# Kernel optimization log

Measured on AMD Instinct MI355X. Metric: run time of the kernel, lower is better.

Reference implementation:

```python
import jax, jax.numpy as jnp
import numpy as np

B, S, H = 2, 1024, 2048
KD = 32
N_CACHE = 16
RANKS = (4, 12, 40, 128)
SIM_THRESH = 0.95
CRIT_T, SIMPLE_T = 0.8, 0.3
EPS = 1e-8


def setup_inputs() -> dict:
    key = jax.random.key(0)
    ks = jax.random.split(key, 24)
    f32 = jnp.float32
    inp = {}
    inp['hidden_states'] = jax.random.normal(ks[0], (B, S, H), f32)
    # token importance scorer: Linear(H, H//4) -> ReLU -> Linear(H//4, 1)
    inp['scorer_w1'] = jax.random.normal(ks[1], (H // 4, H), f32) * 0.1
    inp['scorer_b1'] = jnp.zeros((H // 4,), f32)
    inp['scorer_w2'] = jax.random.normal(ks[2], (1, H // 4), f32) * 0.1
    inp['scorer_b2'] = jnp.zeros((1,), f32)
    inp['pos_importance'] = jnp.ones((1024,), f32)
    # orthogonal key projection [KD, H] (rows orthonormal)
    q, _ = jnp.linalg.qr(jax.random.normal(ks[3], (H, KD), f32))
    inp['key_proj_w'] = q.T
    # cached keys: per-batch-row L2-normalized then flattened, as in _compute_key
    ck = jax.random.normal(ks[4], (N_CACHE, B, KD), f32)
    ck = ck / jnp.linalg.norm(ck, axis=-1, keepdims=True)
    inp['cache_keys'] = ck.reshape(N_CACHE, B * KD)
    inp['cache_deltas'] = jax.random.normal(ks[5], (N_CACHE, B, S, H), f32) * 0.02
    # complexity estimator: Linear(H, 64) -> ReLU -> Linear(64, 4)
    inp['ce_w1'] = jax.random.normal(ks[6], (64, H), f32) * 0.02
    inp['ce_b1'] = jnp.zeros((64,), f32)
    inp['ce_w2'] = jax.random.normal(ks[7], (len(RANKS), 64), f32) * 0.02
    inp['ce_b2'] = jnp.zeros((len(RANKS),), f32)
    # adaptive low-rank U/V per rank option, init std=0.02
    for i, r in enumerate(RANKS):
        inp[f'u{r}'] = jax.random.normal(ks[8 + 2 * i], (r, H), f32) * 0.02
        inp[f'v{r}'] = jax.random.normal(ks[9 + 2 * i], (H, r), f32) * 0.02
    # dense stand-in for the wrapped original transformer layer
    inp['layer_w'] = jax.random.normal(ks[16], (H, H), f32) * 0.02
    inp['layer_b'] = jnp.zeros((H,), f32)
    return inp


def _forward(hidden_states, scorer_w1, scorer_b1, scorer_w2, scorer_b2,
             pos_importance, key_proj_w, cache_keys, cache_deltas,
             ce_w1, ce_b1, ce_w2, ce_b2,
             u4, v4, u12, v12, u40, v40, u128, v128,
             layer_w, layer_b):
    x = hidden_states
    Bn, Sn, _ = x.shape
    # ---- token importance scoring ----
    h = jax.nn.relu(jnp.einsum('bsh,fh->bsf', x, scorer_w1) + scorer_b1)
    content = jnp.einsum('bsf,of->bso', h, scorer_w2)[..., 0] + scorer_b2[0]  # [B,S]
    pos = pos_importance[:Sn][None, :]
    imp = jax.nn.sigmoid(content + 0.1 * pos)
    imp = imp.at[:, 0].multiply(2.0).at[:, -1].multiply(2.0)
    critical = imp > CRIT_T
    simple = imp < SIMPLE_T
    normal = ~(critical | simple)
    # ---- critical path: original layer on critically-masked input ----
    crit_in = jnp.where(critical[..., None], x, 0.0)
    crit_out = jnp.einsum('bsh,oh->bso', crit_in, layer_w) + layer_b
    # ---- simple path: batched 1-NN cosine cache lookup (replaces python loop) ----
    x_pooled = x.mean(axis=1)  # [B,H]
    qk = jax.lax.stop_gradient(x_pooled @ key_proj_w.T)  # no_grad in original
    qk = qk / jnp.maximum(jnp.linalg.norm(qk, axis=-1, keepdims=True), EPS)
    qf = qk.reshape(-1)  # flattened [B*KD], as F.cosine_similarity(dim=0)
    ck = jax.lax.stop_gradient(cache_keys)  # cached entries are detached
    sims = (ck @ qf) / (jnp.maximum(jnp.linalg.norm(ck, axis=-1), EPS)
                        * jnp.maximum(jnp.linalg.norm(qf), EPS))  # [N_CACHE]
    best = jnp.argmax(sims)
    hit = sims[best] >= SIM_THRESH
    cached_delta = jax.lax.stop_gradient(cache_deltas[best])  # [B,S,H]
    lr4 = (x @ u4.T) @ v4.T  # rank-4 update on cache miss
    simple_out = x + jnp.where(hit, cached_delta, lr4)
    # ---- normal path: adaptive-rank low-rank update ----
    ce_h = jax.nn.relu(jax.lax.stop_gradient(x_pooled) @ ce_w1.T + ce_b1)
    scores = ce_h @ ce_w2.T + ce_b2  # [B,4]
    rank_idx = jnp.argmax(scores.reshape(-1)) % len(RANKS)  # flat argmax as torch.argmax
    branches = [
        lambda xx: (xx @ u4.T) @ v4.T,
        lambda xx: (xx @ u12.T) @ v12.T,
        lambda xx: (xx @ u40.T) @ v40.T,
        lambda xx: (xx @ u128.T) @ v128.T,
    ]
    normal_update = jax.lax.switch(rank_idx, branches, x)
    normal_out = x + normal_update
    # ---- route per-token (masks partition all tokens) ----
    out = jnp.where(critical[..., None], crit_out,
          jnp.where(simple[..., None], simple_out, normal_out))
    return out


def reference(hidden_states, scorer_w1, scorer_b1, scorer_w2, scorer_b2,
              pos_importance, key_proj_w, cache_keys, cache_deltas,
              ce_w1, ce_b1, ce_w2, ce_b2,
              u4, v4, u12, v12, u40, v40, u128, v128,
              layer_w, layer_b):
    return _forward(hidden_states, scorer_w1, scorer_b1, scorer_w2, scorer_b2,
                    pos_importance, key_proj_w, cache_keys, cache_deltas,
                    ce_w1, ce_b1, ce_w2, ce_b2,
                    u4, v4, u12, v12, u40, v40, u128, v128,
                    layer_w, layer_b)
```

## Files before the change

### kernel.cpp

```cpp
#include <hip/hip_runtime.h>
#include <math.h>

#define B_  2
#define S_  1024
#define H_  2048
#define F_  512
#define KD_ 32
#define NC_ 16
#define M_  2048
#define NPROJ 184
#define LDP 192
#define KZ_ 4

typedef __attribute__((ext_vector_type(8))) short bf16x8;
typedef __attribute__((ext_vector_type(4))) float f32x4;

typedef __attribute__((address_space(1))) const void gvoid_t;
typedef __attribute__((address_space(3))) void lvoid_t;

__device__ __forceinline__ void gld16(const void* g, void* l) {
    __builtin_amdgcn_global_load_lds((gvoid_t*)g, (lvoid_t*)l, 16, 0, 0);
}

__device__ __forceinline__ ushort f2bf(float f) {
    unsigned u = __float_as_uint(f);
    u += 0x7FFFu + ((u >> 16) & 1u);
    return (ushort)(u >> 16);
}
__device__ __forceinline__ float bf2f(ushort h) {
    return __uint_as_float(((unsigned)h) << 16);
}
__device__ __forceinline__ uint4 pack_hi8(float4 a, float4 b) {
    uint4 r;
    r.x = (unsigned)f2bf(a.x) | ((unsigned)f2bf(a.y) << 16);
    r.y = (unsigned)f2bf(a.z) | ((unsigned)f2bf(a.w) << 16);
    r.z = (unsigned)f2bf(b.x) | ((unsigned)f2bf(b.y) << 16);
    r.w = (unsigned)f2bf(b.z) | ((unsigned)f2bf(b.w) << 16);
    return r;
}
__device__ __forceinline__ void pack_hilo8(float4 a, float4 b, uint4* hi, uint4* lo) {
    float v[8] = {a.x, a.y, a.z, a.w, b.x, b.y, b.z, b.w};
    unsigned h[8], l[8];
#pragma unroll
    for (int i = 0; i < 8; ++i) {
        ushort hh = f2bf(v[i]);
        h[i] = hh;
        l[i] = f2bf(v[i] - bf2f(hh));
    }
    *hi = make_uint4(h[0] | (h[1] << 16), h[2] | (h[3] << 16),
                     h[4] | (h[5] << 16), h[6] | (h[7] << 16));
    *lo = make_uint4(l[0] | (l[1] << 16), l[2] | (l[3] << 16),
                     l[4] | (l[5] << 16), l[6] | (l[7] << 16));
}

__global__ __launch_bounds__(256) void conv_kernel(
    const float* __restrict__ x, const float* __restrict__ lw,
    const float* __restrict__ sw1,
    const float* __restrict__ u4, const float* __restrict__ u12,
    const float* __restrict__ u40, const float* __restrict__ u128,
    ushort* __restrict__ xhi, ushort* __restrict__ xlo,
    ushort* __restrict__ lwh, ushort* __restrict__ swh,
    ushort* __restrict__ swl, ushort* __restrict__ ubh,
    float* __restrict__ partial) {
    int blk = blockIdx.x, tid = threadIdx.x;
    if (blk < 128) {
        int c0 = tid << 3;
        float cs0 = 0.f, cs1 = 0.f, cs2 = 0.f, cs3 = 0.f;
        float cs4 = 0.f, cs5 = 0.f, cs6 = 0.f, cs7 = 0.f;
        for (int r = 0; r < 16; ++r) {
            size_t off = (size_t)(blk * 16 + r) * H_ + c0;
            float4 a = *(const float4*)(x + off);
            float4 b = *(const float4*)(x + off + 4);
            cs0 += a.x; cs1 += a.y; cs2 += a.z; cs3 += a.w;
            cs4 += b.x; cs5 += b.y; cs6 += b.z; cs7 += b.w;
            uint4 hi, lo;
            pack_hilo8(a, b, &hi, &lo);
            *(uint4*)(xhi + off) = hi;
            *(uint4*)(xlo + off) = lo;
        }
        float* pr = partial + (size_t)blk * H_ + c0;
        pr[0] = cs0; pr[1] = cs1; pr[2] = cs2; pr[3] = cs3;
        pr[4] = cs4; pr[5] = cs5; pr[6] = cs6; pr[7] = cs7;
    } else if (blk < 1152) {
        size_t base = (size_t)(blk - 128) * 4096 + (size_t)tid * 16;
#pragma unroll
        for (int q = 0; q < 2; ++q) {
            size_t o = base + q * 8;
            float4 a = *(const float4*)(lw + o);
            float4 b = *(const float4*)(lw + o + 4);
            *(uint4*)(lwh + o) = pack_hi8(a, b);
        }
    } else if (blk < 1408) {
        size_t base = (size_t)(blk - 1152) * 4096 + (size_t)tid * 16;
#pragma unroll
        for (int q = 0; q < 2; ++q) {
            size_t o = base + q * 8;
            float4 a = *(const float4*)(sw1 + o);
            float4 b = *(const float4*)(sw1 + o + 4);
            uint4 hi, lo;
            pack_hilo8(a, b, &hi, &lo);
            *(uint4*)(swh + o) = hi;
            *(uint4*)(swl + o) = lo;
        }
    } else {
        const float* src; ushort* dst; int rel;
        if (blk < 1410)      { src = u4;   dst = ubh;            rel = blk - 1408; }
        else if (blk < 1416) { src = u12;  dst = ubh + 4 * H_;   rel = blk - 1410; }
        else if (blk < 1436) { src = u40;  dst = ubh + 16 * H_;  rel = blk - 1416; }
        else                 { src = u128; dst = ubh + 56 * H_;  rel = blk - 1436; }
        size_t base = (size_t)rel * 4096 + (size_t)tid * 16;
#pragma unroll
        for (int q = 0; q < 2; ++q) {
            size_t o = base + q * 8;
            float4 a = *(const float4*)(src + o);
            float4 b = *(const float4*)(src + o + 4);
            *(uint4*)(dst + o) = pack_hi8(a, b);
        }
    }
}

__global__ __launch_bounds__(256) void pooldots_kernel(
    const float* __restrict__ partial, const float* __restrict__ kpw,
    const float* __restrict__ cw1, float* __restrict__ dots) {
    __shared__ float red[4];
    int o = blockIdx.x, tid = threadIdx.x;
    int b; const float* wr;
    if (o < 64) {
        b = o >> 5;
        wr = kpw + (size_t)(o & 31) * H_;
    } else {
        int o2 = o - 64;
        b = o2 >> 6;
        wr = cw1 + (size_t)(o2 & 63) * H_;
    }
    int k0 = tid << 3;
    float xs0 = 0.f, xs1 = 0.f, xs2 = 0.f, xs3 = 0.f;
    float xs4 = 0.f, xs5 = 0.f, xs6 = 0.f, xs7 = 0.f;
    const float* pb = partial + (size_t)b * 64 * H_ + k0;
    for (int seg = 0; seg < 64; ++seg) {
        float4 p0 = *(const float4*)(pb + (size_t)seg * H_);
        float4 p1 = *(const float4*)(pb + (size_t)seg * H_ + 4);
        xs0 += p0.x; xs1 += p0.y; xs2 += p0.z; xs3 += p0.w;
        xs4 += p1.x; xs5 += p1.y; xs6 += p1.z; xs7 += p1.w;
    }
    const float inv = 1.0f / S_;
    float4 wa = *(const float4*)(wr + k0);
    float4 wb = *(const float4*)(wr + k0 + 4);
    float s = (xs0 * inv) * wa.x + (xs1 * inv) * wa.y
            + (xs2 * inv) * wa.z + (xs3 * inv) * wa.w
            + (xs4 * inv) * wb.x + (xs5 * inv) * wb.y
            + (xs6 * inv) * wb.z + (xs7 * inv) * wb.w;
    for (int off = 32; off > 0; off >>= 1) s += __shfl_down(s, off, 64);
    if ((tid & 63) == 0) red[tid >> 6] = s;
    __syncthreads();
    if (tid == 0) dots[o] = red[0] + red[1] + red[2] + red[3];
}

__global__ __launch_bounds__(256) void big_gemm(
    const ushort* __restrict__ xhi, const ushort* __restrict__ xlo,
    const ushort* __restrict__ swh, const ushort* __restrict__ swl,
    const ushort* __restrict__ ubh,
    float* __restrict__ Hp, float* __restrict__ Pp) {
    __shared__ ushort Ah[2][128][32], Al[2][128][32], Bh[2][128][32], Bl[2][128][32];
    int m0 = blockIdx.x << 7;
    int ny = blockIdx.y;
    int kz = blockIdx.z;
    bool split = ny < 4;
    int tid = threadIdx.x;
    int lr = tid >> 2;
    int lc = (tid & 3) << 3;
    int lcs = lc ^ (((lr >> 1) & 3) << 3);

    const ushort* a0p = xhi + (size_t)(m0 + lr) * H_ + lcs;
    const ushort* a1p = a0p + (size_t)64 * H_;
    const ushort* l0p = xlo + (size_t)(m0 + lr) * H_ + lcs;
    const ushort* l1p = l0p + (size_t)64 * H_;
    const ushort* b0p; const ushort* b1p;
    const ushort* c0p = l0p; const ushort* c1p = l1p;
    if (split) {
        b0p = swh + (size_t)(ny * 128 + lr) * H_ + lcs;
        b1p = b0p + (size_t)64 * H_;
        c0p = swl + (size_t)(ny * 128 + lr) * H_ + lcs;
        c1p = c0p + (size_t)64 * H_;
    } else {
        b0p = ubh + (size_t)((ny - 4) * 128 + lr) * H_ + lcs;
        b1p = b0p + (size_t)64 * H_;
    }

    int lane = tid & 63, w = tid >> 6;
    int wm = (w >> 1) << 6, wn = (w & 1) << 6;
    int fr = lane & 15;
    int kb = ((lane >> 4) << 3) ^ (((fr >> 1) & 3) << 3);

    f32x4 zero4 = {0.f, 0.f, 0.f, 0.f};
    f32x4 acc[4][4];
#pragma unroll
    for (int i = 0; i < 4; ++i)
#pragma unroll
        for (int j = 0; j < 4; ++j) acc[i][j] = zero4;

    int kbeg = kz << 9;

#define STAGE_BG(bb, k0)                                                  \
    do {                                                                  \
        gld16(a0p + (k0), &Ah[bb][lr][lc]);                               \
        gld16(a1p + (k0), &Ah[bb][lr + 64][lc]);                          \
        gld16(b0p + (k0), &Bh[bb][lr][lc]);                               \
        gld16(b1p + (k0), &Bh[bb][lr + 64][lc]);                          \
        if (split) {                                                      \
            gld16(l0p + (k0), &Al[bb][lr][lc]);                           \
            gld16(l1p + (k0), &Al[bb][lr + 64][lc]);                      \
            gld16(c0p + (k0), &Bl[bb][lr][lc]);                           \
            gld16(c1p + (k0), &Bl[bb][lr + 64][lc]);                      \
        }                                                                 \
    } while (0)

    STAGE_BG(0, kbeg);
    __syncthreads();
    int cur = 0;
    for (int kt = 0; kt < 16; ++kt) {
        if (kt + 1 < 16) STAGE_BG(cur ^ 1, kbeg + ((kt + 1) << 5));
        bf16x8 ah[4], bh4[4], al4[4], bl4[4];
#pragma unroll
        for (int mt = 0; mt < 4; ++mt)
            ah[mt] = *(const bf16x8*)&Ah[cur][wm + (mt << 4) + fr][kb];
#pragma unroll
        for (int nt = 0; nt < 4; ++nt)
            bh4[nt] = *(const bf16x8*)&Bh[cur][wn + (nt << 4) + fr][kb];
        if (split) {
#pragma unroll
            for (int mt = 0; mt < 4; ++mt)
                al4[mt] = *(const bf16x8*)&Al[cur][wm + (mt << 4) + fr][kb];
#pragma unroll
            for (int nt = 0; nt < 4; ++nt)
                bl4[nt] = *(const bf16x8*)&Bl[cur][wn + (nt << 4) + fr][kb];
        }
#pragma unroll
        for (int mt = 0; mt < 4; ++mt)
#pragma unroll
            for (int nt = 0; nt < 4; ++nt) {
                acc[mt][nt] = __builtin_amdgcn_mfma_f32_16x16x32_bf16(
                    ah[mt], bh4[nt], acc[mt][nt], 0, 0, 0);
                if (split) {
                    acc[mt][nt] = __builtin_amdgcn_mfma_f32_16x16x32_bf16(
                        ah[mt], bl4[nt], acc[mt][nt], 0, 0, 0);
                    acc[mt][nt] = __builtin_amdgcn_mfma_f32_16x16x32_bf16(
                        al4[mt], bh4[nt], acc[mt][nt], 0, 0, 0);
                }
            }
        __syncthreads();
        cur ^= 1;
    }
#undef STAGE_BG

    int orr = (lane >> 4) << 2;
    if (split) {
        float* dst = Hp + (size_t)kz * M_ * F_;
#pragma unroll
        for (int mt = 0; mt < 4; ++mt)
#pragma unroll
            for (int r = 0; r < 4; ++r) {
                int m = m0 + wm + (mt << 4) + orr + r;
                float* cr = dst + (size_t)m * F_ + (ny << 7) + wn;
#pragma unroll
                for (int nt = 0; nt < 4; ++nt)
                    cr[(nt << 4) + fr] = acc[mt][nt][r];
            }
    } else {
        float* dst = Pp + (size_t)kz * M_ * LDP;
        int nb0 = (ny - 4) << 7;
#pragma unroll
        for (int mt = 0; mt < 4; ++mt)
#pragma unroll
            for (int r = 0; r < 4; ++r) {
                int m = m0 + wm + (mt << 4) + orr + r;
                float* cr = dst + (size_t)m * LDP;
#pragma unroll
                for (int nt = 0; nt < 4; ++nt) {
                    int c = nb0 + wn + (nt << 4) + fr;
                    if (c < NPROJ) cr[c] = acc[mt][nt][r];
                }
            }
    }
}

__global__ __launch_bounds__(256) void routefinal_kernel(
    const float* __restrict__ Hp, const float* __restrict__ sb1,
    const float* __restrict__ sw2, const float* __restrict__ sb2,
    const float* __restrict__ pos,
    const float* __restrict__ dots, const float* __restrict__ ck,
    const float* __restrict__ cb1, const float* __restrict__ cw2,
    const float* __restrict__ cb2,
    int* __restrict__ flags, int* __restrict__ route, int* __restrict__ clist) {
    int tid = threadIdx.x;
    if (blockIdx.x < 512) {
        int m = ((int)blockIdx.x << 2) + (tid >> 6);
        int lane = tid & 63;
        const float* h0 = Hp + (size_t)m * F_;
        const float* h1 = h0 + (size_t)M_ * F_;
        const float* h2 = h1 + (size_t)M_ * F_;
        const float* h3 = h2 + (size_t)M_ * F_;
        float s = 0.f;
        for (int f = lane; f < F_; f += 64)
            s += fmaxf(h0[f] + h1[f] + h2[f] + h3[f] + sb1[f], 0.f) * sw2[f];
        for (int off = 32; off > 0; off >>= 1) s += __shfl_down(s, off, 64);
        if (lane == 0) {
            float content = s + sb2[0];
            int si = m & (S_ - 1);
            float imp = 1.0f / (1.0f + expf(-(content + 0.1f * pos[si])));
            if (si == 0 || si == S_ - 1) imp *= 2.0f;
            int rt = (imp > 0.8f) ? 0 : ((imp < 0.3f) ? 1 : 2);
            route[m] = rt;
            if (rt == 0) {
                int idx = atomicAdd(&flags[0], 1);
                clist[idx] = m;
            }
        }
        return;
    }
    __shared__ float qk_s[64], ce_s[128], sims_s[NC_], sc_s[8];
    __shared__ float qn_s;
    if (tid < 64) {
        qk_s[tid]      = dots[tid];
        ce_s[tid]      = fmaxf(dots[64 + tid] + cb1[tid & 63], 0.f);
        ce_s[tid + 64] = fmaxf(dots[128 + tid] + cb1[tid & 63], 0.f);
    }
    __syncthreads();
    if (tid == 0) {
        for (int b = 0; b < B_; ++b) {
            float nn = 0.f;
            for (int d = 0; d < KD_; ++d) { float v = qk_s[b * KD_ + d]; nn += v * v; }
            float den = fmaxf(sqrtf(nn), 1e-8f);
            for (int d = 0; d < KD_; ++d) qk_s[b * KD_ + d] /= den;
        }
        float qn = 0.f;
        for (int i = 0; i < B_ * KD_; ++i) qn += qk_s[i] * qk_s[i];
        qn_s = fmaxf(sqrtf(qn), 1e-8f);
    }
    __syncthreads();
    if (tid < NC_) {
        float dot = 0.f, nn = 0.f;
        for (int i = 0; i < B_ * KD_; ++i) {
            float c = ck[tid * (B_ * KD_) + i];
            dot += c * qk_s[i]; nn += c * c;
        }
        sims_s[tid] = dot / (fmaxf(sqrtf(nn), 1e-8f) * qn_s);
    }
    if (tid >= 32 && tid < 40) {
        int p = tid - 32, b = p >> 2, o = p & 3;
        float v = cb2[o];
        for (int j = 0; j < 64; ++j) v += ce_s[b * 64 + j] * cw2[o * 64 + j];
        sc_s[p] = v;
    }
    __syncthreads();
    if (tid == 0) {
        float bestv = -1e30f; int best = 0;
        for (int n = 0; n < NC_; ++n)
            if (sims_s[n] > bestv) { bestv = sims_s[n]; best = n; }
        flags[2] = (bestv >= 0.95f) ? 1 : 0;
        flags[3] = best;
        float bs = -1e30f; int bi = 0;
        for (int p = 0; p < 8; ++p)
            if (sc_s[p] > bs) { bs = sc_s[p]; bi = p; }
        flags[1] = bi & 3;
    }
}

__global__ __launch_bounds__(256) void critstage2_kernel(
    const ushort* __restrict__ xhi, const ushort* __restrict__ lwh,
    const float* __restrict__ lb,
    const float* __restrict__ x, const float* __restrict__ Pp,
    const float* __restrict__ v4, const float* __restrict__ v12,
    const float* __restrict__ v40, const float* __restrict__ v128,
    const float* __restrict__ cd, const int* __restrict__ flags,
    const int* __restrict__ route, const int* __restrict__ clist,
    float* __restrict__ out) {
    __shared__ __align__(16) char smem[32768];
    int bi = blockIdx.x;
    int tid = threadIdx.x;

    if (bi < 256) {
        ushort* As = (ushort*)smem;
        ushort* Bs = As + 8192;
        int M = flags[0];
        int m0 = (bi >> 4) << 7;
        if (m0 >= M) return;
        int n0 = (bi & 15) << 7;
        int lr = tid >> 2, lc = (tid & 3) << 3;
        int lcs = lc ^ (((lr >> 1) & 3) << 3);

        int gm0 = m0 + lr, gm1 = m0 + lr + 64;
        int ar0 = clist[gm0 < M ? gm0 : (M - 1)];
        int ar1 = clist[gm1 < M ? gm1 : (M - 1)];
        const ushort* a0p = xhi + (size_t)ar0 * H_ + lcs;
        const ushort* a1p = xhi + (size_t)ar1 * H_ + lcs;
        const ushort* b0p = lwh + (size_t)(n0 + lr) * H_ + lcs;
        const ushort* b1p = b0p + (size_t)64 * H_;

        int lane = tid & 63, w = tid >> 6;
        int wm = (w >> 1) << 6, wn = (w & 1) << 6;
        int fr = lane & 15;
        int kb = ((lane >> 4) << 3) ^ (((fr >> 1) & 3) << 3);

        f32x4 zero4 = {0.f, 0.f, 0.f, 0.f};
        f32x4 acc[4][4];
#pragma unroll
        for (int i = 0; i < 4; ++i)
#pragma unroll
            for (int j = 0; j < 4; ++j) acc[i][j] = zero4;

#define STAGE_CG(bb, k0)                                                  \
        do {                                                              \
            gld16(a0p + (k0), &As[(bb) * 4096 + lr * 32 + lc]);           \
            gld16(a1p + (k0), &As[(bb) * 4096 + (lr + 64) * 32 + lc]);    \
            gld16(b0p + (k0), &Bs[(bb) * 4096 + lr * 32 + lc]);           \
            gld16(b1p + (k0), &Bs[(bb) * 4096 + (lr + 64) * 32 + lc]);    \
        } while (0)

        STAGE_CG(0, 0);
        __syncthreads();
        int cur = 0;
        for (int kt = 0; kt < 64; ++kt) {
            if (kt + 1 < 64) STAGE_CG(cur ^ 1, (kt + 1) << 5);
            bf16x8 af[4], bf4[4];
#pragma unroll
            for (int mt = 0; mt < 4; ++mt)
                af[mt] = *(const bf16x8*)&As[cur * 4096 + (wm + (mt << 4) + fr) * 32 + kb];
#pragma unroll
            for (int nt = 0; nt < 4; ++nt)
                bf4[nt] = *(const bf16x8*)&Bs[cur * 4096 + (wn + (nt << 4) + fr) * 32 + kb];
#pragma unroll
            for (int mt = 0; mt < 4; ++mt)
#pragma unroll
                for (int nt = 0; nt < 4; ++nt)
                    acc[mt][nt] = __builtin_amdgcn_mfma_f32_16x16x32_bf16(
                        af[mt], bf4[nt], acc[mt][nt], 0, 0, 0);
            __syncthreads();
            cur ^= 1;
        }
#undef STAGE_CG

        int orr = (lane >> 4) << 2;
#pragma unroll
        for (int mt = 0; mt < 4; ++mt)
#pragma unroll
            for (int r = 0; r < 4; ++r) {
                int m = m0 + wm + (mt << 4) + orr + r;
                if (m < M) {
                    float* cr = out + (size_t)clist[m] * H_;
#pragma unroll
                    for (int nt = 0; nt < 4; ++nt) {
                        int c = n0 + wn + (nt << 4) + fr;
                        cr[c] = acc[mt][nt][r] + lb[c];
                    }
                }
            }
        return;
    }

    float* TsR = (float*)smem;
    float* Ts4 = TsR + 16 * 132;
    int*   rt_s = (int*)(Ts4 + 64);
    int sb = bi - 256;
    int m0 = (sb >> 4) << 4;
    int c0 = (sb & 15) << 7;

    if (tid < 16) rt_s[tid] = route[m0 + tid];
    int r = flags[1];
    const float* V = (r == 0) ? v4 : (r == 1) ? v12 : (r == 2) ? v40 : v128;
    int Kr  = (r == 0) ? 4 : (r == 1) ? 12 : (r == 2) ? 40 : 128;
    int off = (r == 0) ? 0 : (r == 1) ? 4  : (r == 2) ? 16 : 56;
    int hit = flags[2], best = flags[3];

    const float* Pp1 = Pp + (size_t)M_ * LDP;
    const float* Pp2 = Pp1 + (size_t)M_ * LDP;
    const float* Pp3 = Pp2 + (size_t)M_ * LDP;
    for (int idx = tid; idx < 16 * Kr; idx += 256) {
        int i = idx / Kr, j = idx - i * Kr;
        size_t o = (size_t)(m0 + i) * LDP + off + j;
        TsR[i * 132 + j] = Pp[o] + Pp1[o] + Pp2[o] + Pp3[o];
    }
    if (tid < 64) {
        int i = tid >> 2, j = tid & 3;
        size_t o = (size_t)(m0 + i) * LDP + j;
        Ts4[i * 4 + j] = Pp[o] + Pp1[o] + Pp2[o] + Pp3[o];
    }
    __syncthreads();
    bool any1 = false, any2 = false;
#pragma unroll
    for (int i = 0; i < 16; ++i) { any1 |= (rt_s[i] == 1); any2 |= (rt_s[i] == 2); }
    if (!any1 && !any2) return;
    bool need4 = any1 && !hit;

    int c = c0 + (tid & 127);
    int i0 = (tid >> 7) << 3;

    float aR[8];
#pragma unroll
    for (int i = 0; i < 8; ++i) aR[i] = 0.f;
    if (any2) {
        const float* vrow = V + (size_t)c * Kr;
        for (int j = 0; j < Kr; j += 4) {
            const float4 vv = *(const float4*)(vrow + j);
#pragma unroll
            for (int i = 0; i < 8; ++i) {
                const float4 tv = *(const float4*)&TsR[(i0 + i) * 132 + j];
                aR[i] += tv.x * vv.x + tv.y * vv.y + tv.z * vv.z + tv.w * vv.w;
            }
        }
    }
    float a4[8];
    if (need4) {
        const float4 vv = *(const float4*)(v4 + (size_t)c * 4);
#pragma unroll
        for (int i = 0; i < 8; ++i) {
            const float4 tv = *(const float4*)&Ts4[(i0 + i) * 4];
            a4[i] = tv.x * vv.x + tv.y * vv.y + tv.z * vv.z + tv.w * vv.w;
        }
    }
#pragma unroll
    for (int i = 0; i < 8; ++i) {
        int rt = rt_s[i0 + i];
        if (rt == 0) continue;
        size_t o = (size_t)(m0 + i0 + i) * H_ + c;
        float upd;
        if (rt == 1)
            upd = hit ? cd[(size_t)best * (size_t)(M_ * H_) + o] : a4[i];
        else
            upd = aR[i];
        out[o] = x[o] + upd;
    }
}

extern "C" void kernel_launch(void* const* d_in, const int* in_sizes, int n_in,
                              void* d_out, int out_size, void* d_ws, size_t ws_size,
                              hipStream_t stream) {
    const float* x    = (const float*)d_in[0];
    const float* sw1  = (const float*)d_in[1];
    const float* sb1  = (const float*)d_in[2];
    const float* sw2  = (const float*)d_in[3];
    const float* sb2  = (const float*)d_in[4];
    const float* pos  = (const float*)d_in[5];
    const float* kpw  = (const float*)d_in[6];
    const float* ck   = (const float*)d_in[7];
    const float* cd   = (const float*)d_in[8];
    const float* cw1  = (const float*)d_in[9];
    const float* cb1  = (const float*)d_in[10];
    const float* cw2  = (const float*)d_in[11];
    const float* cb2  = (const float*)d_in[12];
    const float* u4   = (const float*)d_in[13];
    const float* v4   = (const float*)d_in[14];
    const float* u12  = (const float*)d_in[15];
    const float* v12  = (const float*)d_in[16];
    const float* u40  = (const float*)d_in[17];
    const float* v40  = (const float*)d_in[18];
    const float* u128 = (const float*)d_in[19];
    const float* v128 = (const float*)d_in[20];
    const float* lw   = (const float*)d_in[21];
    const float* lb   = (const float*)d_in[22];
    float* out = (float*)d_out;

    ushort* xhi = (ushort*)d_ws;
    ushort* xlo = xhi + (size_t)M_ * H_;
    ushort* lwh = xlo + (size_t)M_ * H_;
    ushort* swh = lwh + (size_t)H_ * H_;
    ushort* swl = swh + (size_t)F_ * H_;
    ushort* ubh = swl + (size_t)F_ * H_;
    float* fbase   = (float*)(ubh + (size_t)256 * H_);
    float* partial = fbase;
    float* Pp      = partial + 128 * H_;
    float* Hp      = Pp + (size_t)KZ_ * M_ * LDP;
    float* dots    = Hp + (size_t)KZ_ * M_ * F_;
    int*   flags   = (int*)(dots + 256);
    int*   route   = flags + 8;
    int*   clist   = route + M_;

    hipMemsetAsync(flags, 0, sizeof(int), stream);

    conv_kernel<<<1500, 256, 0, stream>>>(x, lw, sw1, u4, u12, u40, u128,
                                          xhi, xlo, lwh, swh, swl, ubh, partial);
    pooldots_kernel<<<192, 256, 0, stream>>>(partial, kpw, cw1, dots);
    big_gemm<<<dim3(16, 6, KZ_), 256, 0, stream>>>(xhi, xlo, swh, swl, ubh, Hp, Pp);
    routefinal_kernel<<<513, 256, 0, stream>>>(Hp, sb1, sw2, sb2, pos,
                                               dots, ck, cb1, cw2, cb2,
                                               flags, route, clist);
    critstage2_kernel<<<2304, 256, 0, stream>>>(xhi, lwh, lb, x, Pp,
                                                v4, v12, v40, v128,
                                                cd, flags, route, clist, out);
}
```

Baseline: 479.6 us.

## Fold pooldots into big_gemm, drop memset, widen stage-2 low-rank tiles

The memset of the flag word moves into conv_kernel, and the pooled-dot work is folded into big_gemm as an extra grid row (ny==6). Each of those blocks computes three dot outputs, which removes two launches and lets the dot work run alongside the GEMM. The low-rank stage-2 blocks now cover 256 columns instead of 128, halving their count. They also check the route early, so blocks with no work exit before loading the Pp partial sums into shared memory. The trade-off is fewer blocks in stage 2 and a few slower extra blocks in the GEMM grid.

```diff
diff --git a/kernel.cpp b/kernel.cpp
--- a/kernel.cpp
+++ b/kernel.cpp
@@ -61,8 +61,9 @@
     ushort* __restrict__ xhi, ushort* __restrict__ xlo,
     ushort* __restrict__ lwh, ushort* __restrict__ swh,
     ushort* __restrict__ swl, ushort* __restrict__ ubh,
-    float* __restrict__ partial) {
+    float* __restrict__ partial, int* __restrict__ flags) {
     int blk = blockIdx.x, tid = threadIdx.x;
+    if (blk == 0 && tid == 0) flags[0] = 0;
     if (blk < 128) {
         int c0 = tid << 3;
         float cs0 = 0.f, cs1 = 0.f, cs2 = 0.f, cs3 = 0.f;
@@ -119,54 +120,61 @@
     }
 }
 
-__global__ __launch_bounds__(256) void pooldots_kernel(
-    const float* __restrict__ partial, const float* __restrict__ kpw,
-    const float* __restrict__ cw1, float* __restrict__ dots) {
-    __shared__ float red[4];
-    int o = blockIdx.x, tid = threadIdx.x;
-    int b; const float* wr;
-    if (o < 64) {
-        b = o >> 5;
-        wr = kpw + (size_t)(o & 31) * H_;
-    } else {
-        int o2 = o - 64;
-        b = o2 >> 6;
-        wr = cw1 + (size_t)(o2 & 63) * H_;
-    }
-    int k0 = tid << 3;
-    float xs0 = 0.f, xs1 = 0.f, xs2 = 0.f, xs3 = 0.f;
-    float xs4 = 0.f, xs5 = 0.f, xs6 = 0.f, xs7 = 0.f;
-    const float* pb = partial + (size_t)b * 64 * H_ + k0;
-    for (int seg = 0; seg < 64; ++seg) {
-        float4 p0 = *(const float4*)(pb + (size_t)seg * H_);
-        float4 p1 = *(const float4*)(pb + (size_t)seg * H_ + 4);
-        xs0 += p0.x; xs1 += p0.y; xs2 += p0.z; xs3 += p0.w;
-        xs4 += p1.x; xs5 += p1.y; xs6 += p1.z; xs7 += p1.w;
-    }
-    const float inv = 1.0f / S_;
-    float4 wa = *(const float4*)(wr + k0);
-    float4 wb = *(const float4*)(wr + k0 + 4);
-    float s = (xs0 * inv) * wa.x + (xs1 * inv) * wa.y
-            + (xs2 * inv) * wa.z + (xs3 * inv) * wa.w
-            + (xs4 * inv) * wb.x + (xs5 * inv) * wb.y
-            + (xs6 * inv) * wb.z + (xs7 * inv) * wb.w;
-    for (int off = 32; off > 0; off >>= 1) s += __shfl_down(s, off, 64);
-    if ((tid & 63) == 0) red[tid >> 6] = s;
-    __syncthreads();
-    if (tid == 0) dots[o] = red[0] + red[1] + red[2] + red[3];
-}
-
 __global__ __launch_bounds__(256) void big_gemm(
     const ushort* __restrict__ xhi, const ushort* __restrict__ xlo,
     const ushort* __restrict__ swh, const ushort* __restrict__ swl,
     const ushort* __restrict__ ubh,
-    float* __restrict__ Hp, float* __restrict__ Pp) {
+    const float* __restrict__ partial, const float* __restrict__ kpw,
+    const float* __restrict__ cw1,
+    float* __restrict__ Hp, float* __restrict__ Pp, float* __restrict__ dots) {
     __shared__ ushort Ah[2][128][32], Al[2][128][32], Bh[2][128][32], Bl[2][128][32];
-    int m0 = blockIdx.x << 7;
+    __shared__ float red_s[4];
     int ny = blockIdx.y;
     int kz = blockIdx.z;
+    int tid = threadIdx.x;
+
+    if (ny == 6) {
+        int idx = ((int)blockIdx.x << 2) | kz;
+        int k0 = tid << 3;
+        const float inv = 1.0f / S_;
+#pragma unroll
+        for (int t = 0; t < 3; ++t) {
+            int o = idx + t * 64;
+            int b; const float* wr;
+            if (o < 64) {
+                b = o >> 5;
+                wr = kpw + (size_t)(o & 31) * H_;
+            } else {
+                int o2 = o - 64;
+                b = o2 >> 6;
+                wr = cw1 + (size_t)(o2 & 63) * H_;
+            }
+            float xs0 = 0.f, xs1 = 0.f, xs2 = 0.f, xs3 = 0.f;
+            float xs4 = 0.f, xs5 = 0.f, xs6 = 0.f, xs7 = 0.f;
+            const float* pb = partial + (size_t)b * 64 * H_ + k0;
+            for (int seg = 0; seg < 64; ++seg) {
+                float4 p0 = *(const float4*)(pb + (size_t)seg * H_);
+                float4 p1 = *(const float4*)(pb + (size_t)seg * H_ + 4);
+                xs0 += p0.x; xs1 += p0.y; xs2 += p0.z; xs3 += p0.w;
+                xs4 += p1.x; xs5 += p1.y; xs6 += p1.z; xs7 += p1.w;
+            }
+            float4 wa = *(const float4*)(wr + k0);
+            float4 wb = *(const float4*)(wr + k0 + 4);
+            float s = (xs0 * inv) * wa.x + (xs1 * inv) * wa.y
+                    + (xs2 * inv) * wa.z + (xs3 * inv) * wa.w
+                    + (xs4 * inv) * wb.x + (xs5 * inv) * wb.y
+                    + (xs6 * inv) * wb.z + (xs7 * inv) * wb.w;
+            for (int off = 32; off > 0; off >>= 1) s += __shfl_down(s, off, 64);
+            __syncthreads();
+            if ((tid & 63) == 0) red_s[tid >> 6] = s;
+            __syncthreads();
+            if (tid == 0) dots[o] = red_s[0] + red_s[1] + red_s[2] + red_s[3];
+        }
+        return;
+    }
+
+    int m0 = blockIdx.x << 7;
     bool split = ny < 4;
-    int tid = threadIdx.x;
     int lr = tid >> 2;
     int lc = (tid & 3) << 3;
     int lcs = lc ^ (((lr >> 1) & 3) << 3);
@@ -462,73 +470,80 @@
     float* Ts4 = TsR + 16 * 132;
     int*   rt_s = (int*)(Ts4 + 64);
     int sb = bi - 256;
-    int m0 = (sb >> 4) << 4;
-    int c0 = (sb & 15) << 7;
+    int m0 = (sb >> 3) << 4;
+    int c0 = (sb & 7) << 8;
 
     if (tid < 16) rt_s[tid] = route[m0 + tid];
+    __syncthreads();
+    bool any1 = false, any2 = false;
+#pragma unroll
+    for (int i = 0; i < 16; ++i) { any1 |= (rt_s[i] == 1); any2 |= (rt_s[i] == 2); }
+    if (!any1 && !any2) return;
+
     int r = flags[1];
     const float* V = (r == 0) ? v4 : (r == 1) ? v12 : (r == 2) ? v40 : v128;
     int Kr  = (r == 0) ? 4 : (r == 1) ? 12 : (r == 2) ? 40 : 128;
     int off = (r == 0) ? 0 : (r == 1) ? 4  : (r == 2) ? 16 : 56;
     int hit = flags[2], best = flags[3];
+    bool need4 = any1 && !hit;
 
     const float* Pp1 = Pp + (size_t)M_ * LDP;
     const float* Pp2 = Pp1 + (size_t)M_ * LDP;
     const float* Pp3 = Pp2 + (size_t)M_ * LDP;
-    for (int idx = tid; idx < 16 * Kr; idx += 256) {
-        int i = idx / Kr, j = idx - i * Kr;
-        size_t o = (size_t)(m0 + i) * LDP + off + j;
-        TsR[i * 132 + j] = Pp[o] + Pp1[o] + Pp2[o] + Pp3[o];
-    }
-    if (tid < 64) {
+    if (any2) {
+        for (int idx = tid; idx < 16 * Kr; idx += 256) {
+            int i = idx / Kr, j = idx - i * Kr;
+            size_t o = (size_t)(m0 + i) * LDP + off + j;
+            TsR[i * 132 + j] = Pp[o] + Pp1[o] + Pp2[o] + Pp3[o];
+        }
+    }
+    if (need4 && tid < 64) {
         int i = tid >> 2, j = tid & 3;
         size_t o = (size_t)(m0 + i) * LDP + j;
         Ts4[i * 4 + j] = Pp[o] + Pp1[o] + Pp2[o] + Pp3[o];
     }
     __syncthreads();
-    bool any1 = false, any2 = false;
-#pragma unroll
-    for (int i = 0; i < 16; ++i) { any1 |= (rt_s[i] == 1); any2 |= (rt_s[i] == 2); }
-    if (!any1 && !any2) return;
-    bool need4 = any1 && !hit;
-
-    int c = c0 + (tid & 127);
+
     int i0 = (tid >> 7) << 3;
-
-    float aR[8];
-#pragma unroll
-    for (int i = 0; i < 8; ++i) aR[i] = 0.f;
-    if (any2) {
-        const float* vrow = V + (size_t)c * Kr;
-        for (int j = 0; j < Kr; j += 4) {
-            const float4 vv = *(const float4*)(vrow + j);
+#pragma unroll
+    for (int hseg = 0; hseg < 2; ++hseg) {
+        int c = c0 + (hseg << 7) + (tid & 127);
+
+        float aR[8];
+#pragma unroll
+        for (int i = 0; i < 8; ++i) aR[i] = 0.f;
+        if (any2) {
+            const float* vrow = V + (size_t)c * Kr;
+            for (int j = 0; j < Kr; j += 4) {
+                const float4 vv = *(const float4*)(vrow + j);
+#pragma unroll
+                for (int i = 0; i < 8; ++i) {
+                    const float4 tv = *(const float4*)&TsR[(i0 + i) * 132 + j];
+                    aR[i] += tv.x * vv.x + tv.y * vv.y + tv.z * vv.z + tv.w * vv.w;
+                }
+            }
+        }
+        float a4[8];
+        if (need4) {
+            const float4 vv = *(const float4*)(v4 + (size_t)c * 4);
 #pragma unroll
             for (int i = 0; i < 8; ++i) {
-                const float4 tv = *(const float4*)&TsR[(i0 + i) * 132 + j];
-                aR[i] += tv.x * vv.x + tv.y * vv.y + tv.z * vv.z + tv.w * vv.w;
-            }
-        }
-    }
-    float a4[8];
-    if (need4) {
-        const float4 vv = *(const float4*)(v4 + (size_t)c * 4);
+                const float4 tv = *(const float4*)&Ts4[(i0 + i) * 4];
+                a4[i] = tv.x * vv.x + tv.y * vv.y + tv.z * vv.z + tv.w * vv.w;
+            }
+        }
 #pragma unroll
         for (int i = 0; i < 8; ++i) {
-            const float4 tv = *(const float4*)&Ts4[(i0 + i) * 4];
-            a4[i] = tv.x * vv.x + tv.y * vv.y + tv.z * vv.z + tv.w * vv.w;
-        }
-    }
-#pragma unroll
-    for (int i = 0; i < 8; ++i) {
-        int rt = rt_s[i0 + i];
-        if (rt == 0) continue;
-        size_t o = (size_t)(m0 + i0 + i) * H_ + c;
-        float upd;
-        if (rt == 1)
-            upd = hit ? cd[(size_t)best * (size_t)(M_ * H_) + o] : a4[i];
-        else
-            upd = aR[i];
-        out[o] = x[o] + upd;
+            int rt = rt_s[i0 + i];
+            if (rt == 0) continue;
+            size_t o = (size_t)(m0 + i0 + i) * H_ + c;
+            float upd;
+            if (rt == 1)
+                upd = hit ? cd[(size_t)best * (size_t)(M_ * H_) + o] : a4[i];
+            else
+                upd = aR[i];
+            out[o] = x[o] + upd;
+        }
     }
 }
 
@@ -575,16 +590,16 @@
     int*   route   = flags + 8;
     int*   clist   = route + M_;
 
-    hipMemsetAsync(flags, 0, sizeof(int), stream);
-
     conv_kernel<<<1500, 256, 0, stream>>>(x, lw, sw1, u4, u12, u40, u128,
-                                          xhi, xlo, lwh, swh, swl, ubh, partial);
-    pooldots_kernel<<<192, 256, 0, stream>>>(partial, kpw, cw1, dots);
-    big_gemm<<<dim3(16, 6, KZ_), 256, 0, stream>>>(xhi, xlo, swh, swl, ubh, Hp, Pp);
+                                          xhi, xlo, lwh, swh, swl, ubh,
+                                          partial, flags);
+    big_gemm<<<dim3(16, 7, KZ_), 256, 0, stream>>>(xhi, xlo, swh, swl, ubh,
+                                                   partial, kpw, cw1,
+                                                   Hp, Pp, dots);
     routefinal_kernel<<<513, 256, 0, stream>>>(Hp, sb1, sw2, sb2, pos,
                                                dots, ck, cb1, cw2, cb2,
                                                flags, route, clist);
-    critstage2_kernel<<<2304, 256, 0, stream>>>(xhi, lwh, lb, x, Pp,
+    critstage2_kernel<<<1280, 256, 0, stream>>>(xhi, lwh, lb, x, Pp,
                                                 v4, v12, v40, v128,
                                                 cd, flags, route, clist, out);
 }
```

Result: no change. 486.5 us (+1.4%).
